# Kernel optimization log

Hardware: AMD Instinct MI355X
Metric: run time of the kernel (lower is better)

## Reference

```python
import jax, jax.numpy as jnp
import numpy as np

IMG, PATCH, CIN, EMB, B = 384, 16, 3, 768, 64
EPS = 1e-4
OCC_THRES = 0.5


def setup_inputs() -> dict:
    key = jax.random.key(0)
    k = jax.random.split(key, 6)
    x = jax.random.normal(k[0], (B, CIN, IMG, IMG), jnp.float32)
    x2 = jax.random.normal(k[1], (B, CIN, IMG, IMG), jnp.float32)

    def mkbox(u):  # normalized [x, y, w, h], guaranteed in-bounds, >=3 feature cells
        xy = 0.05 + 0.45 * u[:, :2]
        wh = 0.15 + 0.25 * u[:, 2:]
        return jnp.concatenate([xy, wh], axis=1)

    gt_patch1 = mkbox(jax.random.uniform(k[2], (B, 4), jnp.float32))
    gt_patch2 = mkbox(jax.random.uniform(k[3], (B, 4), jnp.float32))
    fan_in = CIN * PATCH * PATCH
    W = jax.random.normal(k[4], (EMB, CIN, PATCH, PATCH), jnp.float32) / np.sqrt(fan_in)
    b = jax.random.normal(k[5], (EMB,), jnp.float32) * 0.01
    return {"x": x, "x2": x2, "gt_patch1": gt_patch1, "gt_patch2": gt_patch2, "W": W, "b": b}


def _proj(x, W, b):
    y = jax.lax.conv_general_dilated(
        x, W, window_strides=(PATCH, PATCH), padding='VALID',
        dimension_numbers=('NCHW', 'OIHW', 'NCHW'))
    return y + b[None, :, None, None]


def cal_occ(b1, b2):
    int_xmin = jnp.maximum(b1[:, 0], b2[:, 0])
    int_ymin = jnp.maximum(b1[:, 1], b2[:, 1])
    int_xmax = jnp.minimum(b1[:, 2], b2[:, 2])
    int_ymax = jnp.minimum(b1[:, 3], b2[:, 3])
    int_vol = jnp.clip(int_ymax - int_ymin, 0.0) * jnp.clip(int_xmax - int_xmin, 0.0)
    vol1 = (b1[:, 2] - b1[:, 0]) * (b1[:, 3] - b1[:, 1])
    return (int_vol + 1e-8) / (vol1 + 1e-8)


def _box_mask(box, H, Wd):
    # box [B,4] = (x0,y0,x2,y2) in feature coords; region feat[:, y0:y2, x0:x2)
    yy = jnp.arange(H, dtype=box.dtype)[None, :, None]
    xx = jnp.arange(Wd, dtype=box.dtype)[None, None, :]
    x0 = box[:, 0, None, None]; y0 = box[:, 1, None, None]
    x2 = box[:, 2, None, None]; y2 = box[:, 3, None, None]
    return ((xx >= x0) & (xx < x2) & (yy >= y0) & (yy < y2)).astype(box.dtype)


def _channel_stats(feat, mask):
    # feat [B,C,H,W], mask [B,H,W]; per-channel masked mean / unbiased std (torch .std)
    m = mask[:, None]
    n = jnp.sum(m, axis=(2, 3), keepdims=True)
    mean = jnp.sum(feat * m, axis=(2, 3), keepdims=True) / jnp.maximum(n, 1.0)
    var = jnp.sum(((feat - mean) ** 2) * m, axis=(2, 3), keepdims=True) / jnp.maximum(n - 1.0, 1.0)
    return jax.lax.stop_gradient(mean), jax.lax.stop_gradient(jnp.sqrt(var))


def _update_bbox(b1, b2):
    x0, y0, x2, y2 = b1[:, 0], b1[:, 1], b1[:, 2], b1[:, 3]
    q0, q1, q2, q3 = b2[:, 0], b2[:, 1], b2[:, 2], b2[:, 3]
    condA = (x0 >= q0) & (x2 <= q2)
    subA1 = (q1 <= y0) & (q3 > y0)
    a1 = condA & subA1
    a2 = condA & ~subA1 & (q3 >= y2) & (q1 < y2)
    condB = ~condA & (y0 >= q1) & (y2 <= q3)
    subB1 = (q0 <= x0) & (q2 > x0)
    bb1 = condB & subB1
    bb2 = condB & ~subB1 & (q2 >= x2) & (q0 < x2)
    ny0 = jnp.where(a1, q3, y0)
    ny2 = jnp.where(a2, q1, y2)
    nx0 = jnp.where(bb1, q2, x0)
    nx2 = jnp.where(bb2, q0, x2)
    return jnp.stack([nx0, ny0, nx2, ny2], axis=1)


def reference(x, x2, gt_patch1, gt_patch2, W, b):
    w_ori = x.shape[-1]
    f1 = _proj(x, W, b)   # [B, E, fs, fs]
    f2 = _proj(x2, W, b)
    fs = f1.shape[2]
    patch_sz = w_ori // f1.shape[-1]
    g1 = gt_patch1 * w_ori
    g2 = gt_patch2 * w_ori
    g1 = jnp.concatenate([g1[:, :2], g1[:, :2] + g1[:, 2:] - 1.0], axis=1)
    g2 = jnp.concatenate([g2[:, :2], g2[:, :2] + g2[:, 2:] - 1.0], axis=1)
    g1 = jnp.round(g1 / patch_sz)
    g2 = jnp.round(g2 / patch_sz)
    occ1 = cal_occ(g1, g2)
    occ2 = cal_occ(g2, g1)
    fsf = jnp.asarray(fs, g1.dtype)
    skip1 = ((occ1 > OCC_THRES) | (g2[:, 3] <= g2[:, 1]) | (g2[:, 2] <= g2[:, 0])
             | (g2[:, 0] < 0) | (g2[:, 1] < 0) | (g2[:, 0] >= fsf) | (g2[:, 1] >= fsf))
    skip2 = ((occ2 > OCC_THRES) | (g1[:, 3] <= g1[:, 1]) | (g1[:, 2] <= g1[:, 0])
             | (g1[:, 0] < 0) | (g1[:, 1] < 0) | (g1[:, 0] >= fsf) | (g1[:, 1] >= fsf))
    m1 = _box_mask(g1, fs, fs)
    m2 = _box_mask(g2, fs, fs)
    mean1, std1 = _channel_stats(f1, m1)  # stats of x  in box1
    mean2, std2 = _channel_stats(f2, m2)  # stats of x2 in box2
    # stream 1: paste box2 region of x2 into x with channel mean/std matching
    blend1 = (f2 - mean2) / (std2 + EPS) * (std1 + EPS) + mean1
    out1 = jnp.where(skip1[:, None, None, None], f1,
                     jnp.where(m2[:, None] > 0, blend1, f1))
    # stream 2: paste box1 region of x into x2
    blend2 = (f1 - mean1) / (std1 + EPS) * (std2 + EPS) + mean2
    out2 = jnp.where(skip2[:, None, None, None], f2,
                     jnp.where(m1[:, None] > 0, blend2, f2))
    g1n = jnp.where(skip1[:, None], g1, _update_bbox(g1, g2))
    g2n = jnp.where(skip2[:, None], g2, _update_bbox(g2, g1))
    g1n = jnp.concatenate([g1n[:, :2], g1n[:, 2:] - g1n[:, :2]], axis=1)
    g2n = jnp.concatenate([g2n[:, :2], g2n[:, 2:] - g2n[:, :2]], axis=1)
    Bn, E = out1.shape[0], out1.shape[1]
    o1 = out1.reshape(Bn, E, fs * fs).transpose(0, 2, 1)  # [B, N, E]
    o2 = out2.reshape(Bn, E, fs * fs).transpose(0, 2, 1)
    return (o1, o2, g1n, g2n)
```

## Files before the change

kernel.cpp:

```cpp
#include <hip/hip_runtime.h>
#include <hip/hip_bf16.h>

#define FS 24
#define NPATCH 576
#define EMBD 768
#define KDIM 768
#define NB 64
#define IMGW 384
#define MTOT (NB*NPATCH)
#define EPSV 1e-4f

#define O2_OFS (MTOT*EMBD)
#define G1_OFS (2*O2_OFS)
#define G2_OFS (G1_OFS + NB*4)

#define WS_G1 0
#define WS_G2 256
#define WS_SK1 512
#define WS_SK2 576
#define WS_MEAN1 1024
#define WS_STD1 (WS_MEAN1 + NB*EMBD)
#define WS_MEAN2 (WS_STD1 + NB*EMBD)
#define WS_STD2 (WS_MEAN2 + NB*EMBD)

#define WSB_W  1048576ULL
#define WS_NEED (WSB_W + 1179648ULL)

typedef __attribute__((ext_vector_type(8))) short bf16x8;
typedef __attribute__((ext_vector_type(4))) unsigned short u16x4;
typedef __attribute__((ext_vector_type(8))) unsigned short u16x8;
typedef __attribute__((ext_vector_type(4))) float f32x4;

__device__ __forceinline__ u16x4 cvt4_bf16(f32x4 v) {
    u16x4 r;
#pragma unroll
    for (int j = 0; j < 4; ++j) r[j] = __builtin_bit_cast(unsigned short, (__bf16)v[j]);
    return r;
}

__device__ __forceinline__ bf16x8 cvt8_bf16(f32x4 lo, f32x4 hi) {
    u16x4 a = cvt4_bf16(lo), b = cvt4_bf16(hi);
    u16x8 v;
#pragma unroll
    for (int q = 0; q < 4; ++q) { v[q] = a[q]; v[q+4] = b[q]; }
    return __builtin_bit_cast(bf16x8, v);
}

__device__ __forceinline__ void gload16(const void* g, const void* l) {
    __builtin_amdgcn_global_load_lds(
        (const __attribute__((address_space(1))) unsigned int*)g,
        (__attribute__((address_space(3))) unsigned int*)l, 16, 0, 0);
}

__device__ inline float occ_of(const float b1[4], const float b2[4]) {
    float ixmin = fmaxf(b1[0], b2[0]);
    float iymin = fmaxf(b1[1], b2[1]);
    float ixmax = fminf(b1[2], b2[2]);
    float iymax = fminf(b1[3], b2[3]);
    float iv = fmaxf(iymax - iymin, 0.f) * fmaxf(ixmax - ixmin, 0.f);
    float v1 = (b1[2] - b1[0]) * (b1[3] - b1[1]);
    return (iv + 1e-8f) / (v1 + 1e-8f);
}

__device__ inline void upd_box(const float* b1, const float* b2, float* o) {
    float x0 = b1[0], y0 = b1[1], x2 = b1[2], y2 = b1[3];
    float q0 = b2[0], q1 = b2[1], q2 = b2[2], q3 = b2[3];
    bool condA = (x0 >= q0) && (x2 <= q2);
    bool subA1 = (q1 <= y0) && (q3 > y0);
    bool a1 = condA && subA1;
    bool a2 = condA && !subA1 && (q3 >= y2) && (q1 < y2);
    bool condB = !condA && (y0 >= q1) && (y2 <= q3);
    bool subB1 = (q0 <= x0) && (q2 > x0);
    bool bb1 = condB && subB1;
    bool bb2 = condB && !subB1 && (q2 >= x2) && (q0 < x2);
    o[1] = a1 ? q3 : y0;
    o[3] = a2 ? q1 : y2;
    o[0] = bb1 ? q2 : x0;
    o[2] = bb2 ? q0 : x2;
}

__global__ void boxes_kernel(const float* __restrict__ gt1, const float* __restrict__ gt2,
                             float* __restrict__ gout1, float* __restrict__ gout2,
                             float* __restrict__ ws) {
    const int b = threadIdx.x;
    if (b >= NB) return;
    float g1[4], g2[4];
    {
        float p0 = gt1[b*4+0]*(float)IMGW, p1 = gt1[b*4+1]*(float)IMGW;
        float p2 = gt1[b*4+2]*(float)IMGW, p3 = gt1[b*4+3]*(float)IMGW;
        g1[0] = rintf(p0 / 16.f);
        g1[1] = rintf(p1 / 16.f);
        g1[2] = rintf((p0 + p2 - 1.f) / 16.f);
        g1[3] = rintf((p1 + p3 - 1.f) / 16.f);
    }
    {
        float p0 = gt2[b*4+0]*(float)IMGW, p1 = gt2[b*4+1]*(float)IMGW;
        float p2 = gt2[b*4+2]*(float)IMGW, p3 = gt2[b*4+3]*(float)IMGW;
        g2[0] = rintf(p0 / 16.f);
        g2[1] = rintf(p1 / 16.f);
        g2[2] = rintf((p0 + p2 - 1.f) / 16.f);
        g2[3] = rintf((p1 + p3 - 1.f) / 16.f);
    }
    float occ1 = occ_of(g1, g2), occ2 = occ_of(g2, g1);
    const float fsf = (float)FS;
    bool skip1 = (occ1 > 0.5f) || (g2[3] <= g2[1]) || (g2[2] <= g2[0]) ||
                 (g2[0] < 0.f) || (g2[1] < 0.f) || (g2[0] >= fsf) || (g2[1] >= fsf);
    bool skip2 = (occ2 > 0.5f) || (g1[3] <= g1[1]) || (g1[2] <= g1[0]) ||
                 (g1[0] < 0.f) || (g1[1] < 0.f) || (g1[0] >= fsf) || (g1[1] >= fsf);

    float n1[4], n2[4];
    upd_box(g1, g2, n1);
    upd_box(g2, g1, n2);
    if (skip1) { n1[0]=g1[0]; n1[1]=g1[1]; n1[2]=g1[2]; n1[3]=g1[3]; }
    if (skip2) { n2[0]=g2[0]; n2[1]=g2[1]; n2[2]=g2[2]; n2[3]=g2[3]; }

    gout1[b*4+0] = n1[0]; gout1[b*4+1] = n1[1];
    gout1[b*4+2] = n1[2] - n1[0]; gout1[b*4+3] = n1[3] - n1[1];
    gout2[b*4+0] = n2[0]; gout2[b*4+1] = n2[1];
    gout2[b*4+2] = n2[2] - n2[0]; gout2[b*4+3] = n2[3] - n2[1];

#pragma unroll
    for (int i = 0; i < 4; ++i) { ws[WS_G1 + b*4 + i] = g1[i]; ws[WS_G2 + b*4 + i] = g2[i]; }
    ws[WS_SK1 + b] = skip1 ? 1.f : 0.f;
    ws[WS_SK2 + b] = skip2 ? 1.f : 0.f;
}

__global__ void cvt_w_kernel(const float* __restrict__ Wm, unsigned short* __restrict__ Wb) {
    const int idx = blockIdx.x * 256 + threadIdx.x;
    const f32x4 a = *reinterpret_cast<const f32x4*>(Wm + idx*8);
    const f32x4 b = *reinterpret_cast<const f32x4*>(Wm + idx*8 + 4);
    u16x8 r;
    u16x4 lo = cvt4_bf16(a), hi = cvt4_bf16(b);
#pragma unroll
    for (int j = 0; j < 4; ++j) { r[j] = lo[j]; r[j+4] = hi[j]; }
    *reinterpret_cast<u16x8*>(Wb + idx*8) = r;
}

__global__ __launch_bounds__(256, 3)
void gemm_direct_kernel(const float* __restrict__ x1, const float* __restrict__ xx2,
                        const unsigned short* __restrict__ Wb,
                        const float* __restrict__ bias,
                        float* __restrict__ out) {
    __shared__ __align__(16) unsigned char ldsA[32768];
    __shared__ __align__(16) unsigned char ldsB[16384];

    const float* __restrict__ xin = blockIdx.y ? xx2 : x1;
    float* __restrict__ oo = out + (size_t)blockIdx.y * (size_t)O2_OFS;

    const int bx = blockIdx.x;
    const int swz = (bx & 7) * 216 + (bx >> 3);
    const int mt = swz / 6;
    const int nt = swz - mt * 6;
    const int m0 = mt * 128;
    const int n0 = nt * 128;

    const int tid = threadIdx.x;

    int aoff[8];
    {
        const int pos = tid & 15;
#pragma unroll
        for (int j = 0; j < 8; ++j) {
            const int row = (tid >> 4) + j*16;
            const int m = m0 + row;
            const int bb = m / NPATCH;
            const int p  = m - bb*NPATCH;
            const int py = p / FS, px = p - py*FS;
            const int cs = (pos & 8) | ((pos ^ row) & 7);
            aoff[j] = ((bb*3)*IMGW + py*16 + (cs >> 2)) * IMGW + px*16 + (cs & 3)*4;
        }
    }
    int boff[4];
    {
        const int posb = tid & 7;
#pragma unroll
        for (int j = 0; j < 4; ++j) {
            const int row = (tid >> 3) + j*32;
            boff[j] = (n0 + row)*KDIM + ((posb ^ (row & 7)) << 3);
        }
    }
    const int ldsuni = (tid & 192) * 16;

    f32x4 acc[4][4];
#pragma unroll
    for (int i = 0; i < 4; ++i)
#pragma unroll
        for (int j = 0; j < 4; ++j) acc[i][j] = (f32x4){0.f, 0.f, 0.f, 0.f};

    const int l  = tid & 63;
    const int wid = tid >> 6;
    const int wr = wid >> 1, wc = wid & 1;
    const int fr = l & 15, fq = l >> 4;

#pragma unroll
    for (int kt = 0; kt < 12; ++kt) {
        const int dA = (kt >> 2)*(IMGW*IMGW) + (kt & 3)*(4*IMGW);
        __syncthreads();
#pragma unroll
        for (int j = 0; j < 8; ++j)
            gload16(xin + aoff[j] + dA, ldsA + ldsuni + j*4096);
#pragma unroll
        for (int j = 0; j < 4; ++j)
            gload16(Wb + boff[j] + kt*64, ldsB + ldsuni + j*4096);
        __syncthreads();

#pragma unroll
        for (int ko = 0; ko < 2; ++ko) {
            bf16x8 af[4];
#pragma unroll
            for (int mi = 0; mi < 4; ++mi) {
                const int r = wr*64 + mi*16 + fr;
                const int base = r*256 + ko*128;
                const f32x4 lo = *reinterpret_cast<const f32x4*>(
                    ldsA + base + (((fq*2 + 0) ^ (r & 7)) << 4));
                const f32x4 hi = *reinterpret_cast<const f32x4*>(
                    ldsA + base + (((fq*2 + 1) ^ (r & 7)) << 4));
                af[mi] = cvt8_bf16(lo, hi);
            }
            bf16x8 bfv[4];
#pragma unroll
            for (int ni = 0; ni < 4; ++ni) {
                const int rn = wc*64 + ni*16 + fr;
                bfv[ni] = *reinterpret_cast<const bf16x8*>(
                    ldsB + rn*128 + (((ko*4 + fq) ^ (rn & 7)) << 4));
            }
            __builtin_amdgcn_s_setprio(1);
#pragma unroll
            for (int mi = 0; mi < 4; ++mi)
#pragma unroll
                for (int ni = 0; ni < 4; ++ni)
                    acc[mi][ni] = __builtin_amdgcn_mfma_f32_16x16x32_bf16(
                        af[mi], bfv[ni], acc[mi][ni], 0, 0, 0);
            __builtin_amdgcn_s_setprio(0);
        }
    }

#pragma unroll
    for (int ni = 0; ni < 4; ++ni) {
        const int col = n0 + wc*64 + ni*16 + fr;
        const float bv = bias[col];
#pragma unroll
        for (int mi = 0; mi < 4; ++mi) {
            const int rowb = m0 + wr*64 + mi*16 + fq*4;
#pragma unroll
            for (int r = 0; r < 4; ++r)
                oo[(size_t)(rowb + r)*EMBD + col] = acc[mi][ni][r] + bv;
        }
    }
}

__global__ __launch_bounds__(256, 2)
void embed_gemm_kernel(const float* __restrict__ x1, const float* __restrict__ xx2,
                       const float* __restrict__ Wm, const float* __restrict__ bias,
                       float* __restrict__ out) {
    __shared__ __align__(16) unsigned char As[128*64*2];
    __shared__ __align__(16) unsigned char Bs[128*64*2];

    const float* __restrict__ xin = blockIdx.y ? xx2 : x1;
    float* __restrict__ oo = out + (size_t)blockIdx.y * (size_t)O2_OFS;

    const int bx = blockIdx.x;
    const int swz = (bx & 7) * (1728/8) + (bx >> 3);
    const int mt = swz / 6;
    const int nt = swz - mt * 6;
    const int m0 = mt * 128;
    const int n0 = nt * 128;

    const int tid = threadIdx.x;

    int boffA[8], boffB[8], lofs[8];
#pragma unroll
    for (int it = 0; it < 8; ++it) {
        const int ci = tid + 256*it;
        const int row = ci >> 4, col4 = ci & 15;
        const int m = m0 + row;
        const int bb = m / NPATCH;
        const int p  = m - bb*NPATCH;
        const int py = p / FS, px = p - py*FS;
        boffA[it] = ((bb*3)*IMGW + py*16 + (col4 >> 2)) * IMGW + px*16 + (col4 & 3)*4;
        boffB[it] = (n0 + row)*KDIM + col4*4;
        lofs[it]  = (ci*8) ^ ((row & 7) << 4);
    }

    f32x4 acc[4][4];
#pragma unroll
    for (int i = 0; i < 4; ++i)
#pragma unroll
        for (int j = 0; j < 4; ++j) acc[i][j] = (f32x4){0.f, 0.f, 0.f, 0.f};

    f32x4 stA[8], stB[8];
#pragma unroll
    for (int it = 0; it < 8; ++it) {
        stA[it] = *reinterpret_cast<const f32x4*>(xin + boffA[it]);
        stB[it] = *reinterpret_cast<const f32x4*>(Wm + boffB[it]);
    }

    const int l  = tid & 63;
    const int wid = tid >> 6;
    const int wr = wid >> 1, wc = wid & 1;
    const int fr = l & 15, fq = l >> 4;
    const int xorv = (fr & 7) << 4;

    for (int kt = 0; kt < 12; ++kt) {
        __syncthreads();
#pragma unroll
        for (int it = 0; it < 8; ++it) {
            *reinterpret_cast<u16x4*>(As + lofs[it]) = cvt4_bf16(stA[it]);
            *reinterpret_cast<u16x4*>(Bs + lofs[it]) = cvt4_bf16(stB[it]);
        }
        if (kt + 1 < 12) {
            const int dA = ((kt+1) >> 2) * (IMGW*IMGW) + ((kt+1) & 3) * (4*IMGW);
            const int dB = (kt+1) * 64;
#pragma unroll
            for (int it = 0; it < 8; ++it) {
                stA[it] = *reinterpret_cast<const f32x4*>(xin + boffA[it] + dA);
                stB[it] = *reinterpret_cast<const f32x4*>(Wm + boffB[it] + dB);
            }
        }
        __syncthreads();
#pragma unroll
        for (int ko = 0; ko < 2; ++ko) {
            const int colb = ko*64 + fq*16;
            bf16x8 af[4], bf4[4];
#pragma unroll
            for (int i = 0; i < 4; ++i) {
                af[i]  = *reinterpret_cast<const bf16x8*>(As + (wr*64 + i*16 + fr)*128 + (colb ^ xorv));
                bf4[i] = *reinterpret_cast<const bf16x8*>(Bs + (wc*64 + i*16 + fr)*128 + (colb ^ xorv));
            }
#pragma unroll
            for (int mi = 0; mi < 4; ++mi)
#pragma unroll
                for (int ni = 0; ni < 4; ++ni)
                    acc[mi][ni] = __builtin_amdgcn_mfma_f32_16x16x32_bf16(
                        af[mi], bf4[ni], acc[mi][ni], 0, 0, 0);
        }
    }

#pragma unroll
    for (int ni = 0; ni < 4; ++ni) {
        const int col = n0 + wc*64 + ni*16 + fr;
        const float bv = bias[col];
#pragma unroll
        for (int mi = 0; mi < 4; ++mi) {
            const int rowb = m0 + wr*64 + mi*16 + fq*4;
#pragma unroll
            for (int r = 0; r < 4; ++r)
                oo[(size_t)(rowb + r)*EMBD + col] = acc[mi][ni][r] + bv;
        }
    }
}

__global__ void stats_kernel(const float* __restrict__ o1, const float* __restrict__ o2,
                             float* __restrict__ ws) {
    const int b = blockIdx.y;
    const int c = blockIdx.x * 256 + threadIdx.x;

    float g1[4], g2[4];
#pragma unroll
    for (int i = 0; i < 4; ++i) { g1[i] = ws[WS_G1 + b*4 + i]; g2[i] = ws[WS_G2 + b*4 + i]; }

    for (int t = 0; t < 2; ++t) {
        const float* f = t ? o2 : o1;
        const float* g = t ? g2 : g1;
        int xlo = max(0, (int)g[0]);
        int xhi = min(FS, (int)g[2]);
        int ylo = max(0, (int)g[1]);
        int yhi = min(FS, (int)g[3]);
        float s = 0.f, ss = 0.f;
        for (int py = ylo; py < yhi; ++py)
            for (int px = xlo; px < xhi; ++px) {
                float v = f[(size_t)(b*NPATCH + py*FS + px)*EMBD + c];
                s += v; ss += v*v;
            }
        int nx = xhi - xlo; if (nx < 0) nx = 0;
        int ny = yhi - ylo; if (ny < 0) ny = 0;
        float n = (float)(nx*ny);
        float mean = s / fmaxf(n, 1.f);
        float var = (ss - 2.f*mean*s + n*mean*mean) / fmaxf(n - 1.f, 1.f);
        float sd = sqrtf(fmaxf(var, 0.f));
        ws[(t ? WS_MEAN2 : WS_MEAN1) + b*EMBD + c] = mean;
        ws[(t ? WS_STD2 : WS_STD1) + b*EMBD + c] = sd;
    }
}

__global__ void blend_kernel(float* __restrict__ o1, float* __restrict__ o2,
                             const float* __restrict__ ws) {
    const int b = blockIdx.y;
    const int p = blockIdx.x;
    const int py = p / FS, px = p - py*FS;
    const float pxf = (float)px, pyf = (float)py;

    const float sk1 = ws[WS_SK1 + b];
    const float sk2 = ws[WS_SK2 + b];
    const bool in1 = (pxf >= ws[WS_G1 + b*4+0]) && (pxf < ws[WS_G1 + b*4+2]) &&
                     (pyf >= ws[WS_G1 + b*4+1]) && (pyf < ws[WS_G1 + b*4+3]);
    const bool in2 = (pxf >= ws[WS_G2 + b*4+0]) && (pxf < ws[WS_G2 + b*4+2]) &&
                     (pyf >= ws[WS_G2 + b*4+1]) && (pyf < ws[WS_G2 + b*4+3]);
    const bool do1 = (sk1 == 0.f) && in2;
    const bool do2 = (sk2 == 0.f) && in1;
    if (!do1 && !do2) return;

    const int c = threadIdx.x * 4;
    const size_t base = (size_t)(b*NPATCH + p)*EMBD + c;
    const f32x4 f1 = *reinterpret_cast<const f32x4*>(o1 + base);
    const f32x4 f2 = *reinterpret_cast<const f32x4*>(o2 + base);
    const f32x4 m1 = *reinterpret_cast<const f32x4*>(ws + WS_MEAN1 + b*EMBD + c);
    const f32x4 s1 = *reinterpret_cast<const f32x4*>(ws + WS_STD1  + b*EMBD + c);
    const f32x4 m2 = *reinterpret_cast<const f32x4*>(ws + WS_MEAN2 + b*EMBD + c);
    const f32x4 s2 = *reinterpret_cast<const f32x4*>(ws + WS_STD2  + b*EMBD + c);

    if (do1) {
        f32x4 r;
#pragma unroll
        for (int j = 0; j < 4; ++j)
            r[j] = (f2[j] - m2[j]) / (s2[j] + EPSV) * (s1[j] + EPSV) + m1[j];
        *reinterpret_cast<f32x4*>(o1 + base) = r;
    }
    if (do2) {
        f32x4 r;
#pragma unroll
        for (int j = 0; j < 4; ++j)
            r[j] = (f1[j] - m1[j]) / (s1[j] + EPSV) * (s2[j] + EPSV) + m2[j];
        *reinterpret_cast<f32x4*>(o2 + base) = r;
    }
}

extern "C" void kernel_launch(void* const* d_in, const int* in_sizes, int n_in,
                              void* d_out, int out_size, void* d_ws, size_t ws_size,
                              hipStream_t stream) {
    const float* x    = (const float*)d_in[0];
    const float* x2   = (const float*)d_in[1];
    const float* gt1  = (const float*)d_in[2];
    const float* gt2  = (const float*)d_in[3];
    const float* Wm   = (const float*)d_in[4];
    const float* bias = (const float*)d_in[5];
    float* out = (float*)d_out;
    float* ws  = (float*)d_ws;

    float* o1 = out;
    float* o2 = out + O2_OFS;
    float* g1n = out + G1_OFS;
    float* g2n = out + G2_OFS;

    boxes_kernel<<<1, 64, 0, stream>>>(gt1, gt2, g1n, g2n, ws);

    if (ws_size >= WS_NEED) {
        unsigned short* Wb = (unsigned short*)((char*)d_ws + WSB_W);
        cvt_w_kernel<<<288, 256, 0, stream>>>(Wm, Wb);
        gemm_direct_kernel<<<dim3(1728, 2), 256, 0, stream>>>(x, x2, Wb, bias, out);
    } else {
        embed_gemm_kernel<<<dim3(1728, 2), 256, 0, stream>>>(x, x2, Wm, bias, out);
    }

    stats_kernel<<<dim3(3, NB), 256, 0, stream>>>(o1, o2, ws);
    blend_kernel<<<dim3(NPATCH, NB), 192, 0, stream>>>(o1, o2, ws);
}
```

Baseline: 229.1 us.

## Widen GEMM N-tile to 256, double-buffer A in LDS, read W from global

```diff
diff --git a/kernel.cpp b/kernel.cpp
--- a/kernel.cpp
+++ b/kernel.cpp
@@ -136,23 +136,22 @@
     *reinterpret_cast<u16x8*>(Wb + idx*8) = r;
 }
 
-__global__ __launch_bounds__(256, 3)
-void gemm_direct_kernel(const float* __restrict__ x1, const float* __restrict__ xx2,
-                        const unsigned short* __restrict__ Wb,
-                        const float* __restrict__ bias,
-                        float* __restrict__ out) {
-    __shared__ __align__(16) unsigned char ldsA[32768];
-    __shared__ __align__(16) unsigned char ldsB[16384];
+__global__ __launch_bounds__(256, 2)
+void gemm_bn256_kernel(const float* __restrict__ x1, const float* __restrict__ xx2,
+                       const unsigned short* __restrict__ Wb,
+                       const float* __restrict__ bias,
+                       float* __restrict__ out) {
+    __shared__ __align__(16) unsigned char ldsA[2*32768];
 
     const float* __restrict__ xin = blockIdx.y ? xx2 : x1;
     float* __restrict__ oo = out + (size_t)blockIdx.y * (size_t)O2_OFS;
 
     const int bx = blockIdx.x;
-    const int swz = (bx & 7) * 216 + (bx >> 3);
-    const int mt = swz / 6;
-    const int nt = swz - mt * 6;
+    const int swz = (bx & 7) * 108 + (bx >> 3);
+    const int mt = swz / 3;
+    const int nt = swz - mt * 3;
     const int m0 = mt * 128;
-    const int n0 = nt * 128;
+    const int n0 = nt * 256;
 
     const int tid = threadIdx.x;
 
@@ -170,74 +169,72 @@
             aoff[j] = ((bb*3)*IMGW + py*16 + (cs >> 2)) * IMGW + px*16 + (cs & 3)*4;
         }
     }
-    int boff[4];
-    {
-        const int posb = tid & 7;
-#pragma unroll
-        for (int j = 0; j < 4; ++j) {
-            const int row = (tid >> 3) + j*32;
-            boff[j] = (n0 + row)*KDIM + ((posb ^ (row & 7)) << 3);
-        }
-    }
     const int ldsuni = (tid & 192) * 16;
 
-    f32x4 acc[4][4];
+    f32x4 acc[4][8];
 #pragma unroll
     for (int i = 0; i < 4; ++i)
 #pragma unroll
-        for (int j = 0; j < 4; ++j) acc[i][j] = (f32x4){0.f, 0.f, 0.f, 0.f};
+        for (int j = 0; j < 8; ++j) acc[i][j] = (f32x4){0.f, 0.f, 0.f, 0.f};
 
     const int l  = tid & 63;
     const int wid = tid >> 6;
     const int wr = wid >> 1, wc = wid & 1;
     const int fr = l & 15, fq = l >> 4;
 
+    const unsigned short* bbase = Wb + (size_t)(n0 + wc*128 + fr)*KDIM + fq*8;
+
+#pragma unroll
+    for (int j = 0; j < 8; ++j)
+        gload16(xin + aoff[j], ldsA + ldsuni + j*4096);
+    __syncthreads();
+
 #pragma unroll
     for (int kt = 0; kt < 12; ++kt) {
-        const int dA = (kt >> 2)*(IMGW*IMGW) + (kt & 3)*(4*IMGW);
-        __syncthreads();
-#pragma unroll
-        for (int j = 0; j < 8; ++j)
-            gload16(xin + aoff[j] + dA, ldsA + ldsuni + j*4096);
-#pragma unroll
-        for (int j = 0; j < 4; ++j)
-            gload16(Wb + boff[j] + kt*64, ldsB + ldsuni + j*4096);
-        __syncthreads();
-
+        const int cur = kt & 1;
+        if (kt + 1 < 12) {
+            const int dA = ((kt+1) >> 2)*(IMGW*IMGW) + ((kt+1) & 3)*(4*IMGW);
+#pragma unroll
+            for (int j = 0; j < 8; ++j)
+                gload16(xin + aoff[j] + dA, ldsA + (cur^1)*32768 + ldsuni + j*4096);
+        }
 #pragma unroll
         for (int ko = 0; ko < 2; ++ko) {
             bf16x8 af[4];
 #pragma unroll
             for (int mi = 0; mi < 4; ++mi) {
                 const int r = wr*64 + mi*16 + fr;
-                const int base = r*256 + ko*128;
+                const int base = cur*32768 + r*256 + ko*128;
                 const f32x4 lo = *reinterpret_cast<const f32x4*>(
                     ldsA + base + (((fq*2 + 0) ^ (r & 7)) << 4));
                 const f32x4 hi = *reinterpret_cast<const f32x4*>(
                     ldsA + base + (((fq*2 + 1) ^ (r & 7)) << 4));
                 af[mi] = cvt8_bf16(lo, hi);
             }
-            bf16x8 bfv[4];
-#pragma unroll
-            for (int ni = 0; ni < 4; ++ni) {
-                const int rn = wc*64 + ni*16 + fr;
-                bfv[ni] = *reinterpret_cast<const bf16x8*>(
-                    ldsB + rn*128 + (((ko*4 + fq) ^ (rn & 7)) << 4));
+            const int kofs = kt*64 + ko*32;
+#pragma unroll
+            for (int n4 = 0; n4 < 2; ++n4) {
+                bf16x8 bfv[4];
+#pragma unroll
+                for (int nj = 0; nj < 4; ++nj)
+                    bfv[nj] = *reinterpret_cast<const bf16x8*>(
+                        bbase + (size_t)(n4*64 + nj*16)*KDIM + kofs);
+                __builtin_amdgcn_s_setprio(1);
+#pragma unroll
+                for (int mi = 0; mi < 4; ++mi)
+#pragma unroll
+                    for (int nj = 0; nj < 4; ++nj)
+                        acc[mi][n4*4 + nj] = __builtin_amdgcn_mfma_f32_16x16x32_bf16(
+                            af[mi], bfv[nj], acc[mi][n4*4 + nj], 0, 0, 0);
+                __builtin_amdgcn_s_setprio(0);
             }
-            __builtin_amdgcn_s_setprio(1);
-#pragma unroll
-            for (int mi = 0; mi < 4; ++mi)
-#pragma unroll
-                for (int ni = 0; ni < 4; ++ni)
-                    acc[mi][ni] = __builtin_amdgcn_mfma_f32_16x16x32_bf16(
-                        af[mi], bfv[ni], acc[mi][ni], 0, 0, 0);
-            __builtin_amdgcn_s_setprio(0);
-        }
-    }
-
-#pragma unroll
-    for (int ni = 0; ni < 4; ++ni) {
-        const int col = n0 + wc*64 + ni*16 + fr;
+        }
+        __syncthreads();
+    }
+
+#pragma unroll
+    for (int ni = 0; ni < 8; ++ni) {
+        const int col = n0 + wc*128 + ni*16 + fr;
         const float bv = bias[col];
 #pragma unroll
         for (int mi = 0; mi < 4; ++mi) {
@@ -447,7 +444,7 @@
     if (ws_size >= WS_NEED) {
         unsigned short* Wb = (unsigned short*)((char*)d_ws + WSB_W);
         cvt_w_kernel<<<288, 256, 0, stream>>>(Wm, Wb);
-        gemm_direct_kernel<<<dim3(1728, 2), 256, 0, stream>>>(x, x2, Wb, bias, out);
+        gemm_bn256_kernel<<<dim3(864, 2), 256, 0, stream>>>(x, x2, Wb, bias, out);
     } else {
         embed_gemm_kernel<<<dim3(1728, 2), 256, 0, stream>>>(x, x2, Wm, bias, out);
     }
```

New measurement: 305.4 us. +33.3%, slower.

## Widen GEMM N-tile to 192 and register-prefetch A with bf16 LDS staging

Applied to the files above, without the earlier changes.

```diff
diff --git a/kernel.cpp b/kernel.cpp
--- a/kernel.cpp
+++ b/kernel.cpp
@@ -38,12 +38,12 @@
     return r;
 }
 
-__device__ __forceinline__ bf16x8 cvt8_bf16(f32x4 lo, f32x4 hi) {
+__device__ __forceinline__ u16x8 cvt8u_bf16(f32x4 lo, f32x4 hi) {
     u16x4 a = cvt4_bf16(lo), b = cvt4_bf16(hi);
     u16x8 v;
 #pragma unroll
     for (int q = 0; q < 4; ++q) { v[q] = a[q]; v[q+4] = b[q]; }
-    return __builtin_bit_cast(bf16x8, v);
+    return v;
 }
 
 __device__ __forceinline__ void gload16(const void* g, const void* l) {
@@ -129,122 +129,128 @@
     const int idx = blockIdx.x * 256 + threadIdx.x;
     const f32x4 a = *reinterpret_cast<const f32x4*>(Wm + idx*8);
     const f32x4 b = *reinterpret_cast<const f32x4*>(Wm + idx*8 + 4);
-    u16x8 r;
-    u16x4 lo = cvt4_bf16(a), hi = cvt4_bf16(b);
-#pragma unroll
-    for (int j = 0; j < 4; ++j) { r[j] = lo[j]; r[j+4] = hi[j]; }
-    *reinterpret_cast<u16x8*>(Wb + idx*8) = r;
+    *reinterpret_cast<u16x8*>(Wb + idx*8) = cvt8u_bf16(a, b);
 }
 
 __global__ __launch_bounds__(256, 3)
-void gemm_direct_kernel(const float* __restrict__ x1, const float* __restrict__ xx2,
-                        const unsigned short* __restrict__ Wb,
-                        const float* __restrict__ bias,
-                        float* __restrict__ out) {
-    __shared__ __align__(16) unsigned char ldsA[32768];
-    __shared__ __align__(16) unsigned char ldsB[16384];
+void gemm_bn192_kernel(const float* __restrict__ x1, const float* __restrict__ xx2,
+                       const unsigned short* __restrict__ Wb,
+                       const float* __restrict__ bias,
+                       float* __restrict__ out) {
+    __shared__ __align__(16) unsigned char ldsA[16384];
+    __shared__ __align__(16) unsigned char ldsB[24576];
 
     const float* __restrict__ xin = blockIdx.y ? xx2 : x1;
     float* __restrict__ oo = out + (size_t)blockIdx.y * (size_t)O2_OFS;
 
     const int bx = blockIdx.x;
-    const int swz = (bx & 7) * 216 + (bx >> 3);
-    const int mt = swz / 6;
-    const int nt = swz - mt * 6;
+    const int swz = (bx & 7) * 144 + (bx >> 3);
+    const int mt = swz >> 2;
+    const int nt = swz & 3;
     const int m0 = mt * 128;
-    const int n0 = nt * 128;
+    const int n0 = nt * 192;
 
     const int tid = threadIdx.x;
 
-    int aoff[8];
-    {
-        const int pos = tid & 15;
-#pragma unroll
-        for (int j = 0; j < 8; ++j) {
-            const int row = (tid >> 4) + j*16;
-            const int m = m0 + row;
-            const int bb = m / NPATCH;
-            const int p  = m - bb*NPATCH;
-            const int py = p / FS, px = p - py*FS;
-            const int cs = (pos & 8) | ((pos ^ row) & 7);
-            aoff[j] = ((bb*3)*IMGW + py*16 + (cs >> 2)) * IMGW + px*16 + (cs & 3)*4;
-        }
-    }
-    int boff[4];
-    {
-        const int posb = tid & 7;
-#pragma unroll
-        for (int j = 0; j < 4; ++j) {
-            const int row = (tid >> 3) + j*32;
-            boff[j] = (n0 + row)*KDIM + ((posb ^ (row & 7)) << 3);
-        }
+    int aoffA[4], lofsA[4];
+#pragma unroll
+    for (int j = 0; j < 4; ++j) {
+        const int ci = tid + 256*j;
+        const int row = ci >> 3, c8 = ci & 7;
+        const int m = m0 + row;
+        const int bb = m / NPATCH;
+        const int p  = m - bb*NPATCH;
+        const int py = p / FS, px = p - py*FS;
+        aoffA[j] = ((bb*3)*IMGW + py*16 + (c8 >> 1)) * IMGW + px*16 + (c8 & 1)*8;
+        lofsA[j] = (ci*16) ^ ((row & 7) << 4);
+    }
+    int boff[6];
+#pragma unroll
+    for (int j = 0; j < 6; ++j) {
+        const int s = tid + j*256;
+        const int row = s >> 3, pos = s & 7;
+        boff[j] = (n0 + row)*KDIM + ((pos ^ (row & 7)) << 3);
     }
     const int ldsuni = (tid & 192) * 16;
 
-    f32x4 acc[4][4];
+    f32x4 acc[4][6];
 #pragma unroll
     for (int i = 0; i < 4; ++i)
 #pragma unroll
-        for (int j = 0; j < 4; ++j) acc[i][j] = (f32x4){0.f, 0.f, 0.f, 0.f};
+        for (int j = 0; j < 6; ++j) acc[i][j] = (f32x4){0.f, 0.f, 0.f, 0.f};
 
     const int l  = tid & 63;
     const int wid = tid >> 6;
     const int wr = wid >> 1, wc = wid & 1;
     const int fr = l & 15, fq = l >> 4;
-
-#pragma unroll
+    const int xorv = (fr & 7) << 4;
+
+    f32x4 LA[4][2];
+
+#pragma unroll
+    for (int j = 0; j < 4; ++j) {
+        LA[j][0] = *reinterpret_cast<const f32x4*>(xin + aoffA[j]);
+        LA[j][1] = *reinterpret_cast<const f32x4*>(xin + aoffA[j] + 4);
+    }
+
     for (int kt = 0; kt < 12; ++kt) {
-        const int dA = (kt >> 2)*(IMGW*IMGW) + (kt & 3)*(4*IMGW);
-        __syncthreads();
-#pragma unroll
-        for (int j = 0; j < 8; ++j)
-            gload16(xin + aoff[j] + dA, ldsA + ldsuni + j*4096);
+        asm volatile("s_barrier" ::: "memory");
 #pragma unroll
         for (int j = 0; j < 4; ++j)
+            *reinterpret_cast<u16x8*>(ldsA + lofsA[j]) = cvt8u_bf16(LA[j][0], LA[j][1]);
+#pragma unroll
+        for (int j = 0; j < 6; ++j)
             gload16(Wb + boff[j] + kt*64, ldsB + ldsuni + j*4096);
-        __syncthreads();
+        if (kt + 1 < 12) {
+            const int dA = ((kt+1) >> 2)*(IMGW*IMGW) + ((kt+1) & 3)*(4*IMGW);
+#pragma unroll
+            for (int j = 0; j < 4; ++j) {
+                LA[j][0] = *reinterpret_cast<const f32x4*>(xin + aoffA[j] + dA);
+                LA[j][1] = *reinterpret_cast<const f32x4*>(xin + aoffA[j] + dA + 4);
+            }
+            asm volatile("s_waitcnt vmcnt(8) lgkmcnt(0)\ns_barrier" ::: "memory");
+        } else {
+            asm volatile("s_waitcnt vmcnt(0) lgkmcnt(0)\ns_barrier" ::: "memory");
+        }
+        __builtin_amdgcn_sched_barrier(0);
 
 #pragma unroll
         for (int ko = 0; ko < 2; ++ko) {
+            const int colb = ko*64 + fq*16;
             bf16x8 af[4];
 #pragma unroll
             for (int mi = 0; mi < 4; ++mi) {
                 const int r = wr*64 + mi*16 + fr;
-                const int base = r*256 + ko*128;
-                const f32x4 lo = *reinterpret_cast<const f32x4*>(
-                    ldsA + base + (((fq*2 + 0) ^ (r & 7)) << 4));
-                const f32x4 hi = *reinterpret_cast<const f32x4*>(
-                    ldsA + base + (((fq*2 + 1) ^ (r & 7)) << 4));
-                af[mi] = cvt8_bf16(lo, hi);
-            }
-            bf16x8 bfv[4];
-#pragma unroll
-            for (int ni = 0; ni < 4; ++ni) {
-                const int rn = wc*64 + ni*16 + fr;
-                bfv[ni] = *reinterpret_cast<const bf16x8*>(
+                af[mi] = *reinterpret_cast<const bf16x8*>(ldsA + r*128 + (colb ^ xorv));
+            }
+            bf16x8 bfv[6];
+#pragma unroll
+            for (int nj = 0; nj < 6; ++nj) {
+                const int rn = wc*96 + nj*16 + fr;
+                bfv[nj] = *reinterpret_cast<const bf16x8*>(
                     ldsB + rn*128 + (((ko*4 + fq) ^ (rn & 7)) << 4));
             }
             __builtin_amdgcn_s_setprio(1);
 #pragma unroll
             for (int mi = 0; mi < 4; ++mi)
 #pragma unroll
-                for (int ni = 0; ni < 4; ++ni)
-                    acc[mi][ni] = __builtin_amdgcn_mfma_f32_16x16x32_bf16(
-                        af[mi], bfv[ni], acc[mi][ni], 0, 0, 0);
+                for (int nj = 0; nj < 6; ++nj)
+                    acc[mi][nj] = __builtin_amdgcn_mfma_f32_16x16x32_bf16(
+                        af[mi], bfv[nj], acc[mi][nj], 0, 0, 0);
             __builtin_amdgcn_s_setprio(0);
         }
     }
 
 #pragma unroll
-    for (int ni = 0; ni < 4; ++ni) {
-        const int col = n0 + wc*64 + ni*16 + fr;
+    for (int nj = 0; nj < 6; ++nj) {
+        const int col = n0 + wc*96 + nj*16 + fr;
         const float bv = bias[col];
 #pragma unroll
         for (int mi = 0; mi < 4; ++mi) {
             const int rowb = m0 + wr*64 + mi*16 + fq*4;
 #pragma unroll
             for (int r = 0; r < 4; ++r)
-                oo[(size_t)(rowb + r)*EMBD + col] = acc[mi][ni][r] + bv;
+                oo[(size_t)(rowb + r)*EMBD + col] = acc[mi][nj][r] + bv;
         }
     }
 }
@@ -447,7 +453,7 @@
     if (ws_size >= WS_NEED) {
         unsigned short* Wb = (unsigned short*)((char*)d_ws + WSB_W);
         cvt_w_kernel<<<288, 256, 0, stream>>>(Wm, Wb);
-        gemm_direct_kernel<<<dim3(1728, 2), 256, 0, stream>>>(x, x2, Wb, bias, out);
+        gemm_bn192_kernel<<<dim3(1152, 2), 256, 0, stream>>>(x, x2, Wb, bias, out);
     } else {
         embed_gemm_kernel<<<dim3(1728, 2), 256, 0, stream>>>(x, x2, Wm, bias, out);
     }
```

After: 507.8 us. +121.7%, slower.
